# Kernel tuning notes

Measured on AMD Instinct MI355X. Metric: run time of the kernel, lower is better.

The kernel has to match this reference:

```python
import jax, jax.numpy as jnp
import numpy as np
import math

IN_DIM, OUT_DIM, NUM_BASIS = 256, 128, 6
MAX_IN_SEQ, MAX_OUT_SEQ = 512, 256
REDUCTION = 2
LN_EPS = 1e-5


def setup_inputs() -> dict:
    key = jax.random.key(0)
    ks = jax.random.split(key, 8)
    u = lambda k, shape, a: jax.random.uniform(k, shape, jnp.float32, -a, a)
    x = jax.random.normal(ks[0], (16, MAX_IN_SEQ, IN_DIM), jnp.float32)
    M = u(ks[1], (OUT_DIM, IN_DIM), 0.5)
    P = u(ks[2], (OUT_DIM, OUT_DIM, NUM_BASIS), 0.1)
    Linker = u(ks[3], (MAX_IN_SEQ, MAX_OUT_SEQ), 0.1)
    ln_gamma = jnp.ones((OUT_DIM,), jnp.float32)
    ln_beta = jnp.zeros((OUT_DIM,), jnp.float32)
    res_W = u(ks[4], (OUT_DIM, IN_DIM), 0.1)
    res_linker = u(ks[5], (MAX_IN_SEQ, MAX_OUT_SEQ), 0.1)
    # periods[i,j,g] = i*(out_dim*num_basis) + j*num_basis + g + 2 (non-trainable buffer)
    periods = (jnp.arange(OUT_DIM * OUT_DIM * NUM_BASIS, dtype=jnp.float32)
               .reshape(OUT_DIM, OUT_DIM, NUM_BASIS) + 2.0)
    return {"x": x, "M": M, "P": P, "Linker": Linker, "ln_gamma": ln_gamma,
            "ln_beta": ln_beta, "res_W": res_W, "res_linker": res_linker,
            "periods": periods, "actual_seq_len": 512}


def _layer_norm(z, gamma, beta):
    mu = jnp.mean(z, axis=-1, keepdims=True)
    var = jnp.var(z, axis=-1, keepdims=True)
    return (z - mu) * jax.lax.rsqrt(var + LN_EPS) * gamma + beta


def reference(x, M, P, Linker, ln_gamma, ln_beta, res_W, res_linker, periods, actual_seq_len):
    b, seq_len, _ = x.shape
    # Z = LN(x @ M^T)
    Z = _layer_norm(jnp.matmul(x, M.T), ln_gamma, ln_beta)  # (b, s, out)
    # position-dependent trig basis: phi[s,i,j,g] = cos(2*pi*s / periods[i,j,g])
    k = jnp.arange(seq_len, dtype=jnp.float32)[:, None, None, None]
    phi = jnp.cos(2.0 * math.pi * k / periods[None])          # (s, out, out, nb)
    # fold basis into per-position mixing matrix, then contract (matches sum over dims 3,4)
    W = jnp.einsum('ijg,sijg->sij', P, phi)                   # (s, out, out)
    T = jnp.einsum('bsj,sij->bsi', Z, W)                      # (b, s, out)
    # adaptive linker: reduce sequence length
    L = actual_seq_len
    Lo = max(1, L // REDUCTION)
    U = jnp.einsum('bsi,so->boi', T[:, :L], Linker[:L, :Lo])  # (b, out_seq, out)
    # 'separate' residual
    rfeat = jnp.matmul(x[:, :L], res_W.T)                     # (b, s, out)
    residual = jnp.einsum('bsi,so->boi', rfeat, res_linker[:L, :Lo])
    return U + residual
```

## Files before the change

kernel.cpp:

```cpp
#include <hip/hip_runtime.h>
#include <hip/hip_bf16.h>

#define LN_EPS 1e-5f

typedef __attribute__((ext_vector_type(8))) short short8;
typedef __attribute__((ext_vector_type(4))) float floatx4;

__device__ __forceinline__ float bf2f(unsigned int u16) {
    union { unsigned int i; float f; } v; v.i = (u16 & 0xffffu) << 16; return v.f;
}
__device__ __forceinline__ unsigned short f2bf(float f) {
    __hip_bfloat16 h = __float2bfloat16(f);
    union { __hip_bfloat16 h; unsigned short u; } v; v.h = h; return v.u;
}
__device__ __forceinline__ unsigned int pack2(float a, float b) {
    return (unsigned int)f2bf(a) | ((unsigned int)f2bf(b) << 16);
}
__device__ __forceinline__ short8 pack8(float4 a, float4 b) {
    union { short8 s; uint4 u; } v;
    v.u.x = pack2(a.x, a.y); v.u.y = pack2(a.z, a.w);
    v.u.z = pack2(b.x, b.y); v.u.w = pack2(b.z, b.w);
    return v.s;
}

__global__ __launch_bounds__(256) void kA_w_lcat(const float* __restrict__ P,
                                                 const float* __restrict__ periods,
                                                 const float* __restrict__ Linker,
                                                 const float* __restrict__ resL,
                                                 unsigned short* __restrict__ W,
                                                 unsigned short* __restrict__ LcatT) {
    __shared__ unsigned short lds[32 * 260];
    int blk = blockIdx.x, t = threadIdx.x;
    if (blk < 512) {
        int et = blk & 31, sc = blk >> 5;
        int e0 = et * 512 + t * 2;
        const float* pp = P + (size_t)e0 * 6;
        float4 pa = *(const float4*)(pp);
        float4 pb = *(const float4*)(pp + 4);
        float4 pc = *(const float4*)(pp + 8);
        float pf[12] = { pa.x, pa.y, pa.z, pa.w, pb.x, pb.y, pb.z, pb.w, pc.x, pc.y, pc.z, pc.w };
        const float* qp = periods + (size_t)e0 * 6;
        float4 qa = *(const float4*)(qp);
        float4 qb = *(const float4*)(qp + 4);
        float4 qc = *(const float4*)(qp + 8);
        float iv[12] = { __builtin_amdgcn_rcpf(qa.x), __builtin_amdgcn_rcpf(qa.y),
                         __builtin_amdgcn_rcpf(qa.z), __builtin_amdgcn_rcpf(qa.w),
                         __builtin_amdgcn_rcpf(qb.x), __builtin_amdgcn_rcpf(qb.y),
                         __builtin_amdgcn_rcpf(qb.z), __builtin_amdgcn_rcpf(qb.w),
                         __builtin_amdgcn_rcpf(qc.x), __builtin_amdgcn_rcpf(qc.y),
                         __builtin_amdgcn_rcpf(qc.z), __builtin_amdgcn_rcpf(qc.w) };
        float s0 = (float)(sc * 32);
        float tc[12], cm1[12], cc[12];
        #pragma unroll
        for (int g = 0; g < 12; ++g) {
            tc[g]  = 2.0f * __builtin_amdgcn_cosf(iv[g]);
            cm1[g] = __builtin_amdgcn_cosf(__builtin_amdgcn_fractf(s0 * iv[g]));
            cc[g]  = __builtin_amdgcn_cosf(__builtin_amdgcn_fractf((s0 + 1.0f) * iv[g]));
        }
        #pragma unroll 4
        for (int ss = 0; ss < 32; ++ss) {
            float a0 = 0.f, a1 = 0.f;
            #pragma unroll
            for (int g = 0; g < 6; ++g)  a0 += pf[g] * cm1[g];
            #pragma unroll
            for (int g = 6; g < 12; ++g) a1 += pf[g] * cm1[g];
            int s = sc * 32 + ss;
            *(unsigned int*)(W + (size_t)s * 16384 + e0) = pack2(a0, a1);
            #pragma unroll
            for (int g = 0; g < 12; ++g) {
                float cn = fmaf(tc[g], cc[g], -cm1[g]);
                cm1[g] = cc[g]; cc[g] = cn;
            }
        }
    } else {
        int kb = blk - 512;
        int k0 = kb * 32;
        const float* src = (kb < 16) ? (Linker + (size_t)k0 * 256)
                                     : (resL + (size_t)(k0 - 512) * 256);
        #pragma unroll
        for (int q = 0; q < 8; ++q) {
            int lin = t + 256 * q;
            int row = lin >> 6, col4 = (lin & 63) * 4;
            float4 v = *(const float4*)(src + row * 256 + col4);
            *(unsigned int*)(lds + row * 260 + col4)     = pack2(v.x, v.y);
            *(unsigned int*)(lds + row * 260 + col4 + 2) = pack2(v.z, v.w);
        }
        __syncthreads();
        int o = t;
        unsigned int outw[16];
        #pragma unroll
        for (int kp = 0; kp < 16; ++kp) {
            unsigned int lo = lds[(2 * kp) * 260 + o];
            unsigned int hi = lds[(2 * kp + 1) * 260 + o];
            outw[kp] = lo | (hi << 16);
        }
        unsigned short* dst = LcatT + (size_t)o * 1024 + k0;
        #pragma unroll
        for (int qq = 0; qq < 4; ++qq) {
            uint4 u; u.x = outw[qq*4]; u.y = outw[qq*4+1]; u.z = outw[qq*4+2]; u.w = outw[qq*4+3];
            *(uint4*)(dst + qq * 8) = u;
        }
    }
}

__global__ __launch_bounds__(256) void k1_zr(const float* __restrict__ x,
                                             const float* __restrict__ M,
                                             const float* __restrict__ resW,
                                             const float* __restrict__ gamma,
                                             const float* __restrict__ beta,
                                             unsigned short* __restrict__ Z,
                                             unsigned short* __restrict__ TRt) {
    __shared__ float buf[32 * 258];
    __shared__ float red1[32 * 8], red2[32 * 8];
    __shared__ float mus[32], rsg[32];
    int t = threadIdx.x, w = t >> 6, l = t & 63;
    int lane15 = l & 15, quad = l >> 4;
    int r0 = blockIdx.x * 32;
    const float* wbase = (w < 2) ? M : resW;
    int wco = (w < 2) ? (w * 64) : (w * 64 - 128);
    floatx4 acc[2][4] = {};
    for (int kk = 0; kk < 256; kk += 32) {
        int k0 = kk + quad * 8;
        const float* xr0 = x + (size_t)(r0 + lane15) * 256 + k0;
        const float* xr1 = x + (size_t)(r0 + 16 + lane15) * 256 + k0;
        short8 a0 = pack8(*(const float4*)xr0, *(const float4*)(xr0 + 4));
        short8 a1 = pack8(*(const float4*)xr1, *(const float4*)(xr1 + 4));
        #pragma unroll
        for (int nt = 0; nt < 4; ++nt) {
            const float* br = wbase + (size_t)(wco + nt * 16 + lane15) * 256 + k0;
            short8 b = pack8(*(const float4*)br, *(const float4*)(br + 4));
            acc[0][nt] = __builtin_amdgcn_mfma_f32_16x16x32_bf16(a0, b, acc[0][nt], 0, 0, 0);
            acc[1][nt] = __builtin_amdgcn_mfma_f32_16x16x32_bf16(a1, b, acc[1][nt], 0, 0, 0);
        }
    }
    #pragma unroll
    for (int mt = 0; mt < 2; ++mt)
        #pragma unroll
        for (int nt = 0; nt < 4; ++nt)
            #pragma unroll
            for (int r = 0; r < 4; ++r) {
                int ro = mt * 16 + quad * 4 + r;
                int co = w * 64 + nt * 16 + lane15;
                buf[ro * 258 + co] = acc[mt][nt][r];
            }
    __syncthreads();
    {
        int r = t >> 3, seg = t & 7;
        float s1 = 0.f, s2 = 0.f;
        #pragma unroll
        for (int e = 0; e < 16; ++e) { float v = buf[r * 258 + seg * 16 + e]; s1 += v; s2 += v * v; }
        red1[r * 8 + seg] = s1; red2[r * 8 + seg] = s2;
    }
    __syncthreads();
    if (t < 32) {
        float s1 = 0.f, s2 = 0.f;
        #pragma unroll
        for (int e = 0; e < 8; ++e) { s1 += red1[t * 8 + e]; s2 += red2[t * 8 + e]; }
        float mu = s1 * (1.0f / 128.0f);
        float var = s2 * (1.0f / 128.0f) - mu * mu;
        mus[t] = mu; rsg[t] = rsqrtf(var + LN_EPS);
    }
    __syncthreads();
    int b = r0 >> 9, s0 = r0 & 511;
    {
        int r = t >> 3, c0 = (t & 7) * 16;
        int grow = r0 + r;
        float mu = mus[r], rs = rsg[r];
        float zv[16];
        #pragma unroll
        for (int e = 0; e < 16; ++e) {
            int j = c0 + e;
            zv[e] = (buf[r * 258 + j] - mu) * rs * gamma[j] + beta[j];
        }
        uint4 oz0, oz1;
        oz0.x = pack2(zv[0], zv[1]);  oz0.y = pack2(zv[2], zv[3]);
        oz0.z = pack2(zv[4], zv[5]);  oz0.w = pack2(zv[6], zv[7]);
        oz1.x = pack2(zv[8], zv[9]);  oz1.y = pack2(zv[10], zv[11]);
        oz1.z = pack2(zv[12], zv[13]); oz1.w = pack2(zv[14], zv[15]);
        *(uint4*)(Z + (size_t)grow * 128 + c0) = oz0;
        *(uint4*)(Z + (size_t)grow * 128 + c0 + 8) = oz1;
    }
    {
        int j = t >> 1, sh = (t & 1) * 16;
        unsigned int ow[8];
        #pragma unroll
        for (int p = 0; p < 8; ++p) {
            float v0 = buf[(sh + 2 * p) * 258 + 128 + j];
            float v1 = buf[(sh + 2 * p + 1) * 258 + 128 + j];
            ow[p] = pack2(v0, v1);
        }
        unsigned short* dst = TRt + ((size_t)b * 128 + j) * 1024 + 512 + s0 + sh;
        uint4 u0; u0.x = ow[0]; u0.y = ow[1]; u0.z = ow[2]; u0.w = ow[3];
        uint4 u1; u1.x = ow[4]; u1.y = ow[5]; u1.z = ow[6]; u1.w = ow[7];
        *(uint4*)(dst) = u0;
        *(uint4*)(dst + 8) = u1;
    }
}

__global__ __launch_bounds__(256) void k2b_t(const unsigned short* __restrict__ W,
                                             const unsigned short* __restrict__ Z,
                                             unsigned short* __restrict__ TRt) {
    int t = threadIdx.x, w = t >> 6, l = t & 63;
    int lane15 = l & 15, quad = l >> 4;
    int s = blockIdx.x;
    int i0w = w * 32;
    floatx4 acc[2] = {};
    #pragma unroll
    for (int kk = 0; kk < 4; ++kk) {
        int k0 = kk * 32 + quad * 8;
        short8 a = *(const short8*)(Z + ((size_t)lane15 * 512 + s) * 128 + k0);
        #pragma unroll
        for (int nt = 0; nt < 2; ++nt) {
            short8 bf = *(const short8*)(W + (size_t)s * 16384 + (i0w + nt * 16 + lane15) * 128 + k0);
            acc[nt] = __builtin_amdgcn_mfma_f32_16x16x32_bf16(a, bf, acc[nt], 0, 0, 0);
        }
    }
    #pragma unroll
    for (int nt = 0; nt < 2; ++nt) {
        int i = i0w + nt * 16 + lane15;
        #pragma unroll
        for (int r = 0; r < 4; ++r) {
            int brow = quad * 4 + r;
            TRt[((size_t)brow * 128 + i) * 1024 + s] = f2bf(acc[nt][r]);
        }
    }
}

__global__ __launch_bounds__(256) void k3_out(const unsigned short* __restrict__ LcatT,
                                              const unsigned short* __restrict__ TRt,
                                              float* __restrict__ out) {
    __shared__ float red[4 * 32 * 64];
    int t = threadIdx.x, w = t >> 6, l = t & 63;
    int lane15 = l & 15, quad = l >> 4;
    int b = blockIdx.x, o0 = blockIdx.y * 32, i0 = blockIdx.z * 64;
    const unsigned short* trb = TRt + (size_t)b * 128 * 1024;
    floatx4 acc[2][4] = {};
    #pragma unroll 2
    for (int kk = 0; kk < 8; ++kk) {
        int k0 = w * 256 + kk * 32 + quad * 8;
        short8 afr0 = *(const short8*)(LcatT + (size_t)(o0 + lane15) * 1024 + k0);
        short8 afr1 = *(const short8*)(LcatT + (size_t)(o0 + 16 + lane15) * 1024 + k0);
        #pragma unroll
        for (int nt = 0; nt < 4; ++nt) {
            short8 bfr = *(const short8*)(trb + (size_t)(i0 + nt * 16 + lane15) * 1024 + k0);
            acc[0][nt] = __builtin_amdgcn_mfma_f32_16x16x32_bf16(afr0, bfr, acc[0][nt], 0, 0, 0);
            acc[1][nt] = __builtin_amdgcn_mfma_f32_16x16x32_bf16(afr1, bfr, acc[1][nt], 0, 0, 0);
        }
    }
    #pragma unroll
    for (int mt = 0; mt < 2; ++mt)
        #pragma unroll
        for (int nt = 0; nt < 4; ++nt)
            #pragma unroll
            for (int r = 0; r < 4; ++r) {
                int ro = mt * 16 + quad * 4 + r;
                int co = nt * 16 + lane15;
                red[(w * 32 + ro) * 64 + co] = acc[mt][nt][r];
            }
    __syncthreads();
    {
        int ro = t >> 3, c0 = (t & 7) * 8;
        float vs[8];
        #pragma unroll
        for (int e = 0; e < 8; ++e) {
            float sum = 0.f;
            #pragma unroll
            for (int ww = 0; ww < 4; ++ww) sum += red[(ww * 32 + ro) * 64 + c0 + e];
            vs[e] = sum;
        }
        float4 o1 = { vs[0], vs[1], vs[2], vs[3] };
        float4 o2 = { vs[4], vs[5], vs[6], vs[7] };
        size_t ob = ((size_t)b * 256 + o0 + ro) * 128 + i0 + c0;
        *(float4*)(out + ob) = o1;
        *(float4*)(out + ob + 4) = o2;
    }
}

extern "C" void kernel_launch(void* const* d_in, const int* in_sizes, int n_in,
                              void* d_out, int out_size, void* d_ws, size_t ws_size,
                              hipStream_t stream) {
    const float* x      = (const float*)d_in[0];
    const float* M      = (const float*)d_in[1];
    const float* P      = (const float*)d_in[2];
    const float* Linker = (const float*)d_in[3];
    const float* gamma  = (const float*)d_in[4];
    const float* beta   = (const float*)d_in[5];
    const float* resW   = (const float*)d_in[6];
    const float* resL   = (const float*)d_in[7];
    const float* periods= (const float*)d_in[8];
    (void)in_sizes; (void)n_in; (void)out_size; (void)ws_size;

    float* ws = (float*)d_ws;
    unsigned short* LcatT = (unsigned short*)(ws);
    unsigned short* Z     = (unsigned short*)(ws + 131072);
    unsigned short* TRt   = (unsigned short*)(ws + 655360);
    unsigned short* W     = (unsigned short*)(ws + 1703936);

    kA_w_lcat<<<544, 256, 0, stream>>>(P, periods, Linker, resL, W, LcatT);
    k1_zr<<<256, 256, 0, stream>>>(x, M, resW, gamma, beta, Z, TRt);
    k2b_t<<<512, 256, 0, stream>>>(W, Z, TRt);
    k3_out<<<dim3(16, 8, 2), 256, 0, stream>>>(LcatT, TRt, (float*)d_out);
}
```

Measured before the change: 121.7 us.

## Fuse four kernels into one cooperative kernel with grid-wide syncs

Merges the W/Linker precompute, the Z/residual GEMM with layernorm, the per-position mixing, and the final linker contraction into a single cooperative kernel of 512 blocks. Two grid.sync() barriers separate the phases, and the phases share one LDS union. The aim is to remove three kernel launch gaps and the tail idle time between launches. In exchange, every block must stay co-resident: occupancy is capped at 2 blocks per CU, grid barriers add cost, and some phases leave blocks idle.

Result: slower. 271.3 us (+123.0%).

```diff
diff --git a/kernel.cpp b/kernel.cpp
--- a/kernel.cpp
+++ b/kernel.cpp
@@ -1,5 +1,8 @@
 #include <hip/hip_runtime.h>
 #include <hip/hip_bf16.h>
+#include <hip/hip_cooperative_groups.h>
+
+namespace cg = cooperative_groups;
 
 #define LN_EPS 1e-5f
 
@@ -23,15 +26,33 @@
     return v.s;
 }
 
-__global__ __launch_bounds__(256) void kA_w_lcat(const float* __restrict__ P,
-                                                 const float* __restrict__ periods,
-                                                 const float* __restrict__ Linker,
-                                                 const float* __restrict__ resL,
-                                                 unsigned short* __restrict__ W,
-                                                 unsigned short* __restrict__ LcatT) {
-    __shared__ unsigned short lds[32 * 260];
+union SMem {
+    struct { float buf[32 * 258]; float red1[256]; float red2[256]; float mus[32]; float rsg[32]; } p1;
+    unsigned short lcat[32 * 260];
+    float red[4 * 32 * 64];
+};
+
+__global__ __launch_bounds__(256, 2) void fused_all(const float* __restrict__ x,
+                                                    const float* __restrict__ M,
+                                                    const float* __restrict__ resW,
+                                                    const float* __restrict__ gamma,
+                                                    const float* __restrict__ beta,
+                                                    const float* __restrict__ P,
+                                                    const float* __restrict__ periods,
+                                                    const float* __restrict__ Linker,
+                                                    const float* __restrict__ resL,
+                                                    unsigned short* __restrict__ Z,
+                                                    unsigned short* __restrict__ TRt,
+                                                    unsigned short* __restrict__ W,
+                                                    unsigned short* __restrict__ LcatT,
+                                                    float* __restrict__ out) {
+    __shared__ SMem sm;
+    cg::grid_group grid = cg::this_grid();
     int blk = blockIdx.x, t = threadIdx.x;
-    if (blk < 512) {
+    int w = t >> 6, l = t & 63;
+    int lane15 = l & 15, quad = l >> 4;
+
+    {
         int et = blk & 31, sc = blk >> 5;
         int e0 = et * 512 + t * 2;
         const float* pp = P + (size_t)e0 * 6;
@@ -49,13 +70,13 @@
                          __builtin_amdgcn_rcpf(qb.z), __builtin_amdgcn_rcpf(qb.w),
                          __builtin_amdgcn_rcpf(qc.x), __builtin_amdgcn_rcpf(qc.y),
                          __builtin_amdgcn_rcpf(qc.z), __builtin_amdgcn_rcpf(qc.w) };
-        float s0 = (float)(sc * 32);
+        float s0f = (float)(sc * 32);
         float tc[12], cm1[12], cc[12];
         #pragma unroll
         for (int g = 0; g < 12; ++g) {
             tc[g]  = 2.0f * __builtin_amdgcn_cosf(iv[g]);
-            cm1[g] = __builtin_amdgcn_cosf(__builtin_amdgcn_fractf(s0 * iv[g]));
-            cc[g]  = __builtin_amdgcn_cosf(__builtin_amdgcn_fractf((s0 + 1.0f) * iv[g]));
+            cm1[g] = __builtin_amdgcn_cosf(__builtin_amdgcn_fractf(s0f * iv[g]));
+            cc[g]  = __builtin_amdgcn_cosf(__builtin_amdgcn_fractf((s0f + 1.0f) * iv[g]));
         }
         #pragma unroll 4
         for (int ss = 0; ss < 32; ++ss) {
@@ -72,8 +93,90 @@
                 cm1[g] = cc[g]; cc[g] = cn;
             }
         }
-    } else {
-        int kb = blk - 512;
+    }
+    if (blk < 256) {
+        int r0 = blk * 32;
+        const float* wbase = (w < 2) ? M : resW;
+        int wco = (w < 2) ? (w * 64) : (w * 64 - 128);
+        floatx4 acc[2][4] = {};
+        for (int kk = 0; kk < 256; kk += 32) {
+            int k0 = kk + quad * 8;
+            const float* xr0 = x + (size_t)(r0 + lane15) * 256 + k0;
+            const float* xr1 = x + (size_t)(r0 + 16 + lane15) * 256 + k0;
+            short8 a0 = pack8(*(const float4*)xr0, *(const float4*)(xr0 + 4));
+            short8 a1 = pack8(*(const float4*)xr1, *(const float4*)(xr1 + 4));
+            #pragma unroll
+            for (int nt = 0; nt < 4; ++nt) {
+                const float* br = wbase + (size_t)(wco + nt * 16 + lane15) * 256 + k0;
+                short8 b = pack8(*(const float4*)br, *(const float4*)(br + 4));
+                acc[0][nt] = __builtin_amdgcn_mfma_f32_16x16x32_bf16(a0, b, acc[0][nt], 0, 0, 0);
+                acc[1][nt] = __builtin_amdgcn_mfma_f32_16x16x32_bf16(a1, b, acc[1][nt], 0, 0, 0);
+            }
+        }
+        #pragma unroll
+        for (int mt = 0; mt < 2; ++mt)
+            #pragma unroll
+            for (int nt = 0; nt < 4; ++nt)
+                #pragma unroll
+                for (int r = 0; r < 4; ++r) {
+                    int ro = mt * 16 + quad * 4 + r;
+                    int co = w * 64 + nt * 16 + lane15;
+                    sm.p1.buf[ro * 258 + co] = acc[mt][nt][r];
+                }
+        __syncthreads();
+        {
+            int r = t >> 3, seg = t & 7;
+            float s1 = 0.f, s2 = 0.f;
+            #pragma unroll
+            for (int e = 0; e < 16; ++e) { float v = sm.p1.buf[r * 258 + seg * 16 + e]; s1 += v; s2 += v * v; }
+            sm.p1.red1[r * 8 + seg] = s1; sm.p1.red2[r * 8 + seg] = s2;
+        }
+        __syncthreads();
+        if (t < 32) {
+            float s1 = 0.f, s2 = 0.f;
+            #pragma unroll
+            for (int e = 0; e < 8; ++e) { s1 += sm.p1.red1[t * 8 + e]; s2 += sm.p1.red2[t * 8 + e]; }
+            float mu = s1 * (1.0f / 128.0f);
+            float var = s2 * (1.0f / 128.0f) - mu * mu;
+            sm.p1.mus[t] = mu; sm.p1.rsg[t] = rsqrtf(var + LN_EPS);
+        }
+        __syncthreads();
+        int b = r0 >> 9, s0 = r0 & 511;
+        {
+            int r = t >> 3, c0 = (t & 7) * 16;
+            int grow = r0 + r;
+            float mu = sm.p1.mus[r], rs = sm.p1.rsg[r];
+            float zv[16];
+            #pragma unroll
+            for (int e = 0; e < 16; ++e) {
+                int j = c0 + e;
+                zv[e] = (sm.p1.buf[r * 258 + j] - mu) * rs * gamma[j] + beta[j];
+            }
+            uint4 oz0, oz1;
+            oz0.x = pack2(zv[0], zv[1]);  oz0.y = pack2(zv[2], zv[3]);
+            oz0.z = pack2(zv[4], zv[5]);  oz0.w = pack2(zv[6], zv[7]);
+            oz1.x = pack2(zv[8], zv[9]);  oz1.y = pack2(zv[10], zv[11]);
+            oz1.z = pack2(zv[12], zv[13]); oz1.w = pack2(zv[14], zv[15]);
+            *(uint4*)(Z + (size_t)grow * 128 + c0) = oz0;
+            *(uint4*)(Z + (size_t)grow * 128 + c0 + 8) = oz1;
+        }
+        {
+            int j = t >> 1, sh = (t & 1) * 16;
+            unsigned int ow[8];
+            #pragma unroll
+            for (int p = 0; p < 8; ++p) {
+                float v0 = sm.p1.buf[(sh + 2 * p) * 258 + 128 + j];
+                float v1 = sm.p1.buf[(sh + 2 * p + 1) * 258 + 128 + j];
+                ow[p] = pack2(v0, v1);
+            }
+            unsigned short* dst = TRt + ((size_t)b * 128 + j) * 1024 + 512 + s0 + sh;
+            uint4 u0; u0.x = ow[0]; u0.y = ow[1]; u0.z = ow[2]; u0.w = ow[3];
+            uint4 u1; u1.x = ow[4]; u1.y = ow[5]; u1.z = ow[6]; u1.w = ow[7];
+            *(uint4*)(dst) = u0;
+            *(uint4*)(dst + 8) = u1;
+        }
+    } else if (blk < 288) {
+        int kb = blk - 256;
         int k0 = kb * 32;
         const float* src = (kb < 16) ? (Linker + (size_t)k0 * 256)
                                      : (resL + (size_t)(k0 - 512) * 256);
@@ -82,16 +185,16 @@
             int lin = t + 256 * q;
             int row = lin >> 6, col4 = (lin & 63) * 4;
             float4 v = *(const float4*)(src + row * 256 + col4);
-            *(unsigned int*)(lds + row * 260 + col4)     = pack2(v.x, v.y);
-            *(unsigned int*)(lds + row * 260 + col4 + 2) = pack2(v.z, v.w);
+            *(unsigned int*)(sm.lcat + row * 260 + col4)     = pack2(v.x, v.y);
+            *(unsigned int*)(sm.lcat + row * 260 + col4 + 2) = pack2(v.z, v.w);
         }
         __syncthreads();
         int o = t;
         unsigned int outw[16];
         #pragma unroll
         for (int kp = 0; kp < 16; ++kp) {
-            unsigned int lo = lds[(2 * kp) * 260 + o];
-            unsigned int hi = lds[(2 * kp + 1) * 260 + o];
+            unsigned int lo = sm.lcat[(2 * kp) * 260 + o];
+            unsigned int hi = sm.lcat[(2 * kp + 1) * 260 + o];
             outw[kp] = lo | (hi << 16);
         }
         unsigned short* dst = LcatT + (size_t)o * 1024 + k0;
@@ -101,178 +204,81 @@
             *(uint4*)(dst + qq * 8) = u;
         }
     }
-}
-
-__global__ __launch_bounds__(256) void k1_zr(const float* __restrict__ x,
-                                             const float* __restrict__ M,
-                                             const float* __restrict__ resW,
-                                             const float* __restrict__ gamma,
-                                             const float* __restrict__ beta,
-                                             unsigned short* __restrict__ Z,
-                                             unsigned short* __restrict__ TRt) {
-    __shared__ float buf[32 * 258];
-    __shared__ float red1[32 * 8], red2[32 * 8];
-    __shared__ float mus[32], rsg[32];
-    int t = threadIdx.x, w = t >> 6, l = t & 63;
-    int lane15 = l & 15, quad = l >> 4;
-    int r0 = blockIdx.x * 32;
-    const float* wbase = (w < 2) ? M : resW;
-    int wco = (w < 2) ? (w * 64) : (w * 64 - 128);
-    floatx4 acc[2][4] = {};
-    for (int kk = 0; kk < 256; kk += 32) {
-        int k0 = kk + quad * 8;
-        const float* xr0 = x + (size_t)(r0 + lane15) * 256 + k0;
-        const float* xr1 = x + (size_t)(r0 + 16 + lane15) * 256 + k0;
-        short8 a0 = pack8(*(const float4*)xr0, *(const float4*)(xr0 + 4));
-        short8 a1 = pack8(*(const float4*)xr1, *(const float4*)(xr1 + 4));
-        #pragma unroll
-        for (int nt = 0; nt < 4; ++nt) {
-            const float* br = wbase + (size_t)(wco + nt * 16 + lane15) * 256 + k0;
-            short8 b = pack8(*(const float4*)br, *(const float4*)(br + 4));
-            acc[0][nt] = __builtin_amdgcn_mfma_f32_16x16x32_bf16(a0, b, acc[0][nt], 0, 0, 0);
-            acc[1][nt] = __builtin_amdgcn_mfma_f32_16x16x32_bf16(a1, b, acc[1][nt], 0, 0, 0);
+
+    grid.sync();
+
+    {
+        int s = blk;
+        int i0w = w * 32;
+        floatx4 acc[2] = {};
+        #pragma unroll
+        for (int kk = 0; kk < 4; ++kk) {
+            int k0 = kk * 32 + quad * 8;
+            short8 a = *(const short8*)(Z + ((size_t)lane15 * 512 + s) * 128 + k0);
+            #pragma unroll
+            for (int nt = 0; nt < 2; ++nt) {
+                short8 bf = *(const short8*)(W + (size_t)s * 16384 + (i0w + nt * 16 + lane15) * 128 + k0);
+                acc[nt] = __builtin_amdgcn_mfma_f32_16x16x32_bf16(a, bf, acc[nt], 0, 0, 0);
+            }
+        }
+        #pragma unroll
+        for (int nt = 0; nt < 2; ++nt) {
+            int i = i0w + nt * 16 + lane15;
+            #pragma unroll
+            for (int r = 0; r < 4; ++r) {
+                int brow = quad * 4 + r;
+                TRt[((size_t)brow * 128 + i) * 1024 + s] = f2bf(acc[nt][r]);
+            }
         }
     }
-    #pragma unroll
-    for (int mt = 0; mt < 2; ++mt)
-        #pragma unroll
-        for (int nt = 0; nt < 4; ++nt)
-            #pragma unroll
-            for (int r = 0; r < 4; ++r) {
-                int ro = mt * 16 + quad * 4 + r;
-                int co = w * 64 + nt * 16 + lane15;
-                buf[ro * 258 + co] = acc[mt][nt][r];
-            }
-    __syncthreads();
-    {
-        int r = t >> 3, seg = t & 7;
-        float s1 = 0.f, s2 = 0.f;
-        #pragma unroll
-        for (int e = 0; e < 16; ++e) { float v = buf[r * 258 + seg * 16 + e]; s1 += v; s2 += v * v; }
-        red1[r * 8 + seg] = s1; red2[r * 8 + seg] = s2;
-    }
-    __syncthreads();
-    if (t < 32) {
-        float s1 = 0.f, s2 = 0.f;
-        #pragma unroll
-        for (int e = 0; e < 8; ++e) { s1 += red1[t * 8 + e]; s2 += red2[t * 8 + e]; }
-        float mu = s1 * (1.0f / 128.0f);
-        float var = s2 * (1.0f / 128.0f) - mu * mu;
-        mus[t] = mu; rsg[t] = rsqrtf(var + LN_EPS);
-    }
-    __syncthreads();
-    int b = r0 >> 9, s0 = r0 & 511;
-    {
-        int r = t >> 3, c0 = (t & 7) * 16;
-        int grow = r0 + r;
-        float mu = mus[r], rs = rsg[r];
-        float zv[16];
-        #pragma unroll
-        for (int e = 0; e < 16; ++e) {
-            int j = c0 + e;
-            zv[e] = (buf[r * 258 + j] - mu) * rs * gamma[j] + beta[j];
-        }
-        uint4 oz0, oz1;
-        oz0.x = pack2(zv[0], zv[1]);  oz0.y = pack2(zv[2], zv[3]);
-        oz0.z = pack2(zv[4], zv[5]);  oz0.w = pack2(zv[6], zv[7]);
-        oz1.x = pack2(zv[8], zv[9]);  oz1.y = pack2(zv[10], zv[11]);
-        oz1.z = pack2(zv[12], zv[13]); oz1.w = pack2(zv[14], zv[15]);
-        *(uint4*)(Z + (size_t)grow * 128 + c0) = oz0;
-        *(uint4*)(Z + (size_t)grow * 128 + c0 + 8) = oz1;
-    }
-    {
-        int j = t >> 1, sh = (t & 1) * 16;
-        unsigned int ow[8];
-        #pragma unroll
-        for (int p = 0; p < 8; ++p) {
-            float v0 = buf[(sh + 2 * p) * 258 + 128 + j];
-            float v1 = buf[(sh + 2 * p + 1) * 258 + 128 + j];
-            ow[p] = pack2(v0, v1);
-        }
-        unsigned short* dst = TRt + ((size_t)b * 128 + j) * 1024 + 512 + s0 + sh;
-        uint4 u0; u0.x = ow[0]; u0.y = ow[1]; u0.z = ow[2]; u0.w = ow[3];
-        uint4 u1; u1.x = ow[4]; u1.y = ow[5]; u1.z = ow[6]; u1.w = ow[7];
-        *(uint4*)(dst) = u0;
-        *(uint4*)(dst + 8) = u1;
-    }
-}
-
-__global__ __launch_bounds__(256) void k2b_t(const unsigned short* __restrict__ W,
-                                             const unsigned short* __restrict__ Z,
-                                             unsigned short* __restrict__ TRt) {
-    int t = threadIdx.x, w = t >> 6, l = t & 63;
-    int lane15 = l & 15, quad = l >> 4;
-    int s = blockIdx.x;
-    int i0w = w * 32;
-    floatx4 acc[2] = {};
-    #pragma unroll
-    for (int kk = 0; kk < 4; ++kk) {
-        int k0 = kk * 32 + quad * 8;
-        short8 a = *(const short8*)(Z + ((size_t)lane15 * 512 + s) * 128 + k0);
-        #pragma unroll
-        for (int nt = 0; nt < 2; ++nt) {
-            short8 bf = *(const short8*)(W + (size_t)s * 16384 + (i0w + nt * 16 + lane15) * 128 + k0);
-            acc[nt] = __builtin_amdgcn_mfma_f32_16x16x32_bf16(a, bf, acc[nt], 0, 0, 0);
-        }
-    }
-    #pragma unroll
-    for (int nt = 0; nt < 2; ++nt) {
-        int i = i0w + nt * 16 + lane15;
-        #pragma unroll
-        for (int r = 0; r < 4; ++r) {
-            int brow = quad * 4 + r;
-            TRt[((size_t)brow * 128 + i) * 1024 + s] = f2bf(acc[nt][r]);
-        }
-    }
-}
-
-__global__ __launch_bounds__(256) void k3_out(const unsigned short* __restrict__ LcatT,
-                                              const unsigned short* __restrict__ TRt,
-                                              float* __restrict__ out) {
-    __shared__ float red[4 * 32 * 64];
-    int t = threadIdx.x, w = t >> 6, l = t & 63;
-    int lane15 = l & 15, quad = l >> 4;
-    int b = blockIdx.x, o0 = blockIdx.y * 32, i0 = blockIdx.z * 64;
-    const unsigned short* trb = TRt + (size_t)b * 128 * 1024;
-    floatx4 acc[2][4] = {};
-    #pragma unroll 2
-    for (int kk = 0; kk < 8; ++kk) {
-        int k0 = w * 256 + kk * 32 + quad * 8;
-        short8 afr0 = *(const short8*)(LcatT + (size_t)(o0 + lane15) * 1024 + k0);
-        short8 afr1 = *(const short8*)(LcatT + (size_t)(o0 + 16 + lane15) * 1024 + k0);
-        #pragma unroll
-        for (int nt = 0; nt < 4; ++nt) {
-            short8 bfr = *(const short8*)(trb + (size_t)(i0 + nt * 16 + lane15) * 1024 + k0);
-            acc[0][nt] = __builtin_amdgcn_mfma_f32_16x16x32_bf16(afr0, bfr, acc[0][nt], 0, 0, 0);
-            acc[1][nt] = __builtin_amdgcn_mfma_f32_16x16x32_bf16(afr1, bfr, acc[1][nt], 0, 0, 0);
-        }
-    }
-    #pragma unroll
-    for (int mt = 0; mt < 2; ++mt)
-        #pragma unroll
-        for (int nt = 0; nt < 4; ++nt)
-            #pragma unroll
-            for (int r = 0; r < 4; ++r) {
-                int ro = mt * 16 + quad * 4 + r;
-                int co = nt * 16 + lane15;
-                red[(w * 32 + ro) * 64 + co] = acc[mt][nt][r];
-            }
-    __syncthreads();
-    {
-        int ro = t >> 3, c0 = (t & 7) * 8;
-        float vs[8];
-        #pragma unroll
-        for (int e = 0; e < 8; ++e) {
-            float sum = 0.f;
-            #pragma unroll
-            for (int ww = 0; ww < 4; ++ww) sum += red[(ww * 32 + ro) * 64 + c0 + e];
-            vs[e] = sum;
-        }
-        float4 o1 = { vs[0], vs[1], vs[2], vs[3] };
-        float4 o2 = { vs[4], vs[5], vs[6], vs[7] };
-        size_t ob = ((size_t)b * 256 + o0 + ro) * 128 + i0 + c0;
-        *(float4*)(out + ob) = o1;
-        *(float4*)(out + ob + 4) = o2;
+
+    grid.sync();
+
+    if (blk < 256) {
+        int b = blk & 15, ot = (blk >> 4) & 7, it = blk >> 7;
+        int o0 = ot * 32, i0 = it * 64;
+        const unsigned short* trb = TRt + (size_t)b * 128 * 1024;
+        floatx4 acc[2][4] = {};
+        #pragma unroll 2
+        for (int kk = 0; kk < 8; ++kk) {
+            int k0 = w * 256 + kk * 32 + quad * 8;
+            short8 afr0 = *(const short8*)(LcatT + (size_t)(o0 + lane15) * 1024 + k0);
+            short8 afr1 = *(const short8*)(LcatT + (size_t)(o0 + 16 + lane15) * 1024 + k0);
+            #pragma unroll
+            for (int nt = 0; nt < 4; ++nt) {
+                short8 bfr = *(const short8*)(trb + (size_t)(i0 + nt * 16 + lane15) * 1024 + k0);
+                acc[0][nt] = __builtin_amdgcn_mfma_f32_16x16x32_bf16(afr0, bfr, acc[0][nt], 0, 0, 0);
+                acc[1][nt] = __builtin_amdgcn_mfma_f32_16x16x32_bf16(afr1, bfr, acc[1][nt], 0, 0, 0);
+            }
+        }
+        __syncthreads();
+        #pragma unroll
+        for (int mt = 0; mt < 2; ++mt)
+            #pragma unroll
+            for (int nt = 0; nt < 4; ++nt)
+                #pragma unroll
+                for (int r = 0; r < 4; ++r) {
+                    int ro = mt * 16 + quad * 4 + r;
+                    int co = nt * 16 + lane15;
+                    sm.red[(w * 32 + ro) * 64 + co] = acc[mt][nt][r];
+                }
+        __syncthreads();
+        {
+            int ro = t >> 3, c0 = (t & 7) * 8;
+            float vs[8];
+            #pragma unroll
+            for (int e = 0; e < 8; ++e) {
+                float sum = 0.f;
+                #pragma unroll
+                for (int ww = 0; ww < 4; ++ww) sum += sm.red[(ww * 32 + ro) * 64 + c0 + e];
+                vs[e] = sum;
+            }
+            float4 o1 = { vs[0], vs[1], vs[2], vs[3] };
+            float4 o2 = { vs[4], vs[5], vs[6], vs[7] };
+            size_t ob = ((size_t)b * 256 + o0 + ro) * 128 + i0 + c0;
+            *(float4*)(out + ob) = o1;
+            *(float4*)(out + ob + 4) = o2;
+        }
     }
 }
 
@@ -295,9 +301,10 @@
     unsigned short* Z     = (unsigned short*)(ws + 131072);
     unsigned short* TRt   = (unsigned short*)(ws + 655360);
     unsigned short* W     = (unsigned short*)(ws + 1703936);
-
-    kA_w_lcat<<<544, 256, 0, stream>>>(P, periods, Linker, resL, W, LcatT);
-    k1_zr<<<256, 256, 0, stream>>>(x, M, resW, gamma, beta, Z, TRt);
-    k2b_t<<<512, 256, 0, stream>>>(W, Z, TRt);
-    k3_out<<<dim3(16, 8, 2), 256, 0, stream>>>(LcatT, TRt, (float*)d_out);
-}
+    float* outp = (float*)d_out;
+
+    void* args[] = { (void*)&x, (void*)&M, (void*)&resW, (void*)&gamma, (void*)&beta,
+                     (void*)&P, (void*)&periods, (void*)&Linker, (void*)&resL,
+                     (void*)&Z, (void*)&TRt, (void*)&W, (void*)&LcatT, (void*)&outp };
+    hipLaunchCooperativeKernel((void*)fused_all, dim3(512), dim3(256), args, 0, stream);
+}
```
